# Performance work log

Hardware: AMD Instinct MI355X
Metric: run time of the kernel (lower is better)

Reference implementation:

```python
import jax, jax.numpy as jnp
import numpy as np

DIM = 1024
LATENT_DIM = 512
NUM_HEADS = 16
HEAD_DIM = DIM // NUM_HEADS
SCALE = HEAD_DIM ** -0.5


def setup_inputs() -> dict:
    key = jax.random.key(0)
    k1, k2, k3, k4, k5 = jax.random.split(key, 5)
    B, xN, zN = 2, 2048, 2048
    x = jax.random.normal(k1, (B, xN, DIM), dtype=jnp.float32)
    z = jax.random.normal(k2, (B, zN, LATENT_DIM), dtype=jnp.float32)
    # torch Linear weights: [out_features, in_features]
    Wq = jax.random.normal(k3, (DIM, DIM), dtype=jnp.float32) * (DIM ** -0.5)
    Wkv = jax.random.normal(k4, (2 * DIM, LATENT_DIM), dtype=jnp.float32) * (LATENT_DIM ** -0.5)
    Wo = jax.random.normal(k5, (DIM, DIM), dtype=jnp.float32) * (DIM ** -0.5)
    return {"x": x, "z": z, "Wq": Wq, "Wkv": Wkv, "Wo": Wo}


def reference(x, z, Wq, Wkv, Wo):
    B, xN, _ = x.shape
    _, zN, _ = z.shape
    # projections (torch Linear: y = x @ W.T)
    Q = (x @ Wq.T).reshape(B, xN, NUM_HEADS, HEAD_DIM)        # [B,xN,H,D]
    KV = (z @ Wkv.T).reshape(B, zN, 2, NUM_HEADS, HEAD_DIM)   # [B,zN,2,H,D]
    K = KV[:, :, 0]                                            # [B,zN,H,D]
    V = KV[:, :, 1]
    attn = jnp.einsum('bqhd,bkhd->bhqk', Q, K) * SCALE         # [B,H,xN,zN]
    attn = jax.nn.softmax(attn, axis=-1)
    O = jnp.einsum('bhqk,bkhd->bqhd', attn, V).reshape(B, xN, DIM)
    return O @ Wo.T
```

## Files before the change

### kernel.cpp

```cpp
#include <hip/hip_runtime.h>
#include <stdint.h>

#define SEQ 2048
#define QSCALE 0.1803368801111244f
#define DEFER_THR 11.5f

typedef __attribute__((ext_vector_type(8))) short bf16x8;
typedef __attribute__((ext_vector_type(4))) short bf16x4;
typedef __attribute__((ext_vector_type(4))) float f32x4;
typedef __attribute__((ext_vector_type(16))) float f32x16;
typedef unsigned short u16;

__device__ __forceinline__ u16 f2bf(float f) {
  union { float f; uint32_t u; } v; v.f = f;
  uint32_t u = v.u;
  u += 0x7fffu + ((u >> 16) & 1u);
  return (u16)(u >> 16);
}

__device__ __forceinline__ float fast_exp2(float x) {
#if __has_builtin(__builtin_amdgcn_exp2f)
  return __builtin_amdgcn_exp2f(x);
#else
  return exp2f(x);
#endif
}

__device__ __forceinline__ uint32_t cvtpk(float a, float b) {
  uint32_t r;
  asm("v_cvt_pk_bf16_f32 %0, %1, %2" : "=v"(r) : "v"(a), "v"(b));
  return r;
}

__device__ __forceinline__ void swap_pair(uint32_t& a, uint32_t& b, int hi) {
  uint32_t ta = (uint32_t)__shfl_xor((int)a, 32);
  uint32_t tb = (uint32_t)__shfl_xor((int)b, 32);
  a = hi ? tb : a;
  b = hi ? b : ta;
}

__device__ __forceinline__ void gload_lds16(const u16* g, u16* l) {
  __builtin_amdgcn_global_load_lds((__attribute__((address_space(1))) void*)g,
                                   (__attribute__((address_space(3))) void*)l,
                                   16, 0, 0);
}

__global__ void cvt5_kernel(const float* __restrict__ x, const float* __restrict__ z,
                            const float* __restrict__ Wq, const float* __restrict__ Wkv,
                            const float* __restrict__ Wo,
                            u16* __restrict__ xb, u16* __restrict__ zb,
                            u16* __restrict__ wqb, u16* __restrict__ wkvb,
                            u16* __restrict__ wob) {
  const int X4 = 1048576, Z4 = 524288, W4 = 262144;
  const int total = X4 + Z4 + 3 * W4;
  int i = blockIdx.x * blockDim.x + threadIdx.x;
  const int stride = gridDim.x * blockDim.x;
  for (; i < total; i += stride) {
    const float* src; u16* dst; int j = i;
    if (j < X4)              { src = x;   dst = xb; }
    else if ((j -= X4) < Z4) { src = z;   dst = zb; }
    else if ((j -= Z4) < W4) { src = Wq;  dst = wqb; }
    else if ((j -= W4) < W4) { src = Wkv; dst = wkvb; }
    else       { j -= W4;      src = Wo;  dst = wob; }
    float4 v = ((const float4*)src)[j];
    bf16x4 o;
    o[0] = (short)f2bf(v.x); o[1] = (short)f2bf(v.y);
    o[2] = (short)f2bf(v.z); o[3] = (short)f2bf(v.w);
    ((bf16x4*)dst)[j] = o;
  }
}

template <int BN, typename CT>
__device__ __forceinline__ void gemm64_body(const u16* __restrict__ A,
                                            const u16* __restrict__ B,
                                            CT* __restrict__ C,
                                            int N, int K, float scale,
                                            int tm, int tn, u16* As, u16* Bs) {
  constexpr int NB = BN / 32;
  const int tid = threadIdx.x;
  const int wid = tid >> 6;
  const int lane = tid & 63;
  const int lg = lane >> 4, lq = lane & 15;
  const int wr = wid >> 1, wc = wid & 1;

  f32x4 acc[4][NB];
#pragma unroll
  for (int m = 0; m < 4; m++)
#pragma unroll
    for (int n = 0; n < NB; n++)
#pragma unroll
      for (int e = 0; e < 4; e++) acc[m][n][e] = 0.f;

  const int r0 = tid >> 3;
  const int c0 = tid & 7;
  const int sc = (c0 ^ (r0 & 7)) * 8;
  const u16* gA = A + (size_t)(tm * 128 + r0) * K + sc;
  const u16* gB = B + (size_t)(tn * BN + r0) * K + sc;
  u16* lA = As + wid * 512;
  u16* lB = Bs + wid * 512;

  for (int k0 = 0; k0 < K; k0 += 64) {
    __syncthreads();
#pragma unroll
    for (int i = 0; i < 4; i++)
      gload_lds16(gA + k0 + (size_t)(32 * i) * K, lA + i * 2048);
#pragma unroll
    for (int i = 0; i < NB; i++)
      gload_lds16(gB + k0 + (size_t)(32 * i) * K, lB + i * 2048);
    __syncthreads();

#pragma unroll
    for (int ks = 0; ks < 2; ks++) {
      const int slot = ((ks * 4 + lg) ^ (lq & 7)) * 8;
      bf16x8 af[4], bfr[NB];
#pragma unroll
      for (int m = 0; m < 4; m++)
        af[m] = *(const bf16x8*)(As + (wr * 64 + m * 16 + lq) * 64 + slot);
#pragma unroll
      for (int n = 0; n < NB; n++)
        bfr[n] = *(const bf16x8*)(Bs + (wc * (BN / 2) + n * 16 + lq) * 64 + slot);
#pragma unroll
      for (int m = 0; m < 4; m++)
#pragma unroll
        for (int n = 0; n < NB; n++)
          acc[m][n] = __builtin_amdgcn_mfma_f32_16x16x32_bf16(af[m], bfr[n], acc[m][n], 0, 0, 0);
    }
  }

#pragma unroll
  for (int m = 0; m < 4; m++) {
    const int row = tm * 128 + wr * 64 + m * 16 + lg * 4;
#pragma unroll
    for (int i = 0; i < 4; i++) {
      CT* cp = C + (size_t)(row + i) * N + tn * BN + wc * (BN / 2) + lq;
#pragma unroll
      for (int n = 0; n < NB; n++) {
        float v = acc[m][n][i] * scale;
        if constexpr (sizeof(CT) == 2) cp[n * 16] = (CT)f2bf(v);
        else                            cp[n * 16] = (CT)v;
      }
    }
  }
}

__global__ __launch_bounds__(256, 3) void qkv_gemm(const u16* __restrict__ xb,
                                                   const u16* __restrict__ zb,
                                                   const u16* __restrict__ Wqb,
                                                   const u16* __restrict__ Wkvb,
                                                   u16* __restrict__ Qb,
                                                   u16* __restrict__ Kb,
                                                   u16* __restrict__ VTb) {
  __shared__ __align__(16) u16 As[128 * 64];
  __shared__ __align__(16) u16 Bs[128 * 64];
  const int bi = blockIdx.x;
  int g = (bi & 7) * 96 + (bi >> 3);
  if (g < 256) {
    gemm64_body<128, u16>(xb, Wqb, Qb, 1024, 1024, QSCALE, g >> 3, g & 7, As, Bs);
  } else if (g < 512) {
    g -= 256;
    gemm64_body<128, u16>(zb, Wkvb, Kb, 1024, 512, 1.f, g >> 3, g & 7, As, Bs);
  } else {
    g -= 512;
    gemm64_body<128, u16>(Wkvb + 1024 * 512, zb, VTb, 4096, 512, 1.f, g >> 5, g & 31, As, Bs);
  }
}

__global__ __launch_bounds__(256) void combine_kernel(const u16* __restrict__ OP,
                                                      const float2* __restrict__ ml,
                                                      u16* __restrict__ Ob) {
  const int i = blockIdx.x * 256 + threadIdx.x;
  const int grow = i >> 7;
  const int h = (i >> 3) & 15;
  const float2 a0 = ml[grow * 16 + h];
  const float2 a1 = ml[4096 * 16 + grow * 16 + h];
  const float M = fmaxf(a0.x, a1.x);
  float w0 = a0.y * fast_exp2(a0.x - M);
  float w1 = a1.y * fast_exp2(a1.x - M);
  const float inv = 1.f / (w0 + w1);
  w0 *= inv; w1 *= inv;
  const bf16x8 p0 = ((const bf16x8*)OP)[i];
  const bf16x8 p1 = ((const bf16x8*)(OP + (size_t)4096 * 1024))[i];
  bf16x8 o;
#pragma unroll
  for (int e = 0; e < 8; e++) {
    union { uint32_t u; float f; } f0, f1;
    f0.u = ((uint32_t)(u16)p0[e]) << 16;
    f1.u = ((uint32_t)(u16)p1[e]) << 16;
    o[e] = (short)f2bf(w0 * f0.f + w1 * f1.f);
  }
  ((bf16x8*)Ob)[i] = o;
}

__global__ __launch_bounds__(256) void o_gemm(const u16* __restrict__ Ob,
                                              const u16* __restrict__ Wob,
                                              float* __restrict__ out) {
  __shared__ __align__(16) u16 As[128 * 64];
  __shared__ __align__(16) u16 Bs[64 * 64];
  const int bi = blockIdx.x;
  const int xcd = bi & 7, j = bi >> 3;
  const int tm = xcd * 4 + (j >> 4);
  const int tn = j & 15;
  gemm64_body<64, float>(Ob, Wob, out, 1024, 1024, 1.f, tm, tn, As, Bs);
}

__global__ __launch_bounds__(256, 4) void attn_kernel(const u16* __restrict__ Q,
                                                      const u16* __restrict__ K,
                                                      const u16* __restrict__ VT,
                                                      u16* __restrict__ OP,
                                                      float2* __restrict__ ml) {
  __shared__ __align__(16) u16 LDS[16384];

  const int tid = threadIdx.x;
  const int wid = tid >> 6;
  const int lane = tid & 63;
  const int l31 = lane & 31;
  const int hi = lane >> 5;

  const int bi = blockIdx.x;
  const int xcd = bi & 7, j = bi >> 3;
  const int qt = j & 15;
  const int s  = (j >> 4) & 1;
  const int bh = xcd + 8 * (j >> 5);
  const int b = bh >> 4, h = bh & 15;
  const int t0 = s * 16;

  const int q0 = qt * 128 + wid * 32;

  bf16x8 qf[4];
  {
    const u16* qp = Q + (size_t)(b * SEQ + q0 + l31) * 1024 + h * 64 + hi * 8;
#pragma unroll
    for (int ks = 0; ks < 4; ks++) qf[ks] = *(const bf16x8*)(qp + ks * 16);
  }

  f32x16 of[2];
#pragma unroll
  for (int d = 0; d < 2; d++)
#pragma unroll
    for (int e = 0; e < 16; e++) of[d][e] = 0.f;
  float m_run = -3.0e38f, l_run = 0.f;

  const char* rdB[4];
#pragma unroll
  for (int ks = 0; ks < 4; ks++)
    rdB[ks] = (const char*)LDS + l31 * 128 + ((((2 * ks + hi) ^ (lane & 7))) << 4);

  const int r0 = tid >> 3;
  const int srcc = ((tid & 7) ^ (r0 & 7)) << 3;
  const u16* gK = K + (size_t)(b * SEQ + r0) * 1024 + h * 64 + srcc;
  const u16* gV = VT + (size_t)(h * 64 + r0) * 4096 + b * SEQ + srcc;
  u16* lK = LDS + wid * 512;
  u16* lV = LDS + 8192 + wid * 512;

  auto stage = [&](int t, int buf) {
    const u16* sk = gK + (size_t)t * 64 * 1024;
    gload_lds16(sk, lK + buf * 4096);
    gload_lds16(sk + (size_t)32 * 1024, lK + buf * 4096 + 2048);
    const u16* sv = gV + t * 64;
    gload_lds16(sv, lV + buf * 4096);
    gload_lds16(sv + (size_t)32 * 4096, lV + buf * 4096 + 2048);
  };

  auto tile_compute = [&](int buf) {
    const int bo = buf * 8192;

    f32x16 sacc[2];
#pragma unroll
    for (int kb = 0; kb < 2; kb++)
#pragma unroll
      for (int e = 0; e < 16; e++) sacc[kb][e] = 0.f;
    __builtin_amdgcn_s_setprio(1);
#pragma unroll
    for (int kb = 0; kb < 2; kb++)
#pragma unroll
      for (int ks = 0; ks < 4; ks++) {
        bf16x8 kf = *(const bf16x8*)(rdB[ks] + bo + kb * 4096);
        sacc[kb] = __builtin_amdgcn_mfma_f32_32x32x16_bf16(kf, qf[ks], sacc[kb], 0, 0, 0);
      }
    __builtin_amdgcn_s_setprio(0);

    float a0 = sacc[0][0], a1 = sacc[0][1], a2 = sacc[0][2], a3 = sacc[0][3];
#pragma unroll
    for (int e = 4; e < 16; e += 4) {
      a0 = fmaxf(a0, sacc[0][e]);     a1 = fmaxf(a1, sacc[0][e + 1]);
      a2 = fmaxf(a2, sacc[0][e + 2]); a3 = fmaxf(a3, sacc[0][e + 3]);
    }
#pragma unroll
    for (int e = 0; e < 16; e += 4) {
      a0 = fmaxf(a0, sacc[1][e]);     a1 = fmaxf(a1, sacc[1][e + 1]);
      a2 = fmaxf(a2, sacc[1][e + 2]); a3 = fmaxf(a3, sacc[1][e + 3]);
    }
    float tmax = fmaxf(fmaxf(a0, a1), fmaxf(a2, a3));
    tmax = fmaxf(tmax, __shfl_xor(tmax, 32));

    if (!__all(tmax <= m_run + DEFER_THR)) {
      const float m_new = fmaxf(m_run, tmax);
      const float esc = fast_exp2(m_run - m_new);
      l_run *= esc;
#pragma unroll
      for (int r = 0; r < 16; r++) {
        const int qof = (r & 3) + 8 * (r >> 2) + 4 * hi;
        const float e = __shfl(esc, qof);
        of[0][r] *= e;
        of[1][r] *= e;
      }
      m_run = m_new;
    }

    float s0 = 0.f, s1 = 0.f, s2 = 0.f, s3 = 0.f;
#pragma unroll
    for (int kb = 0; kb < 2; kb++)
#pragma unroll
      for (int e = 0; e < 16; e += 4) {
        float p0 = fast_exp2(sacc[kb][e] - m_run);
        float p1 = fast_exp2(sacc[kb][e + 1] - m_run);
        float p2 = fast_exp2(sacc[kb][e + 2] - m_run);
        float p3 = fast_exp2(sacc[kb][e + 3] - m_run);
        sacc[kb][e] = p0; sacc[kb][e + 1] = p1; sacc[kb][e + 2] = p2; sacc[kb][e + 3] = p3;
        s0 += p0; s1 += p1; s2 += p2; s3 += p3;
      }
    l_run += (s0 + s1) + (s2 + s3);

    bf16x8 pa[4];
#pragma unroll
    for (int kb = 0; kb < 2; kb++) {
      uint32_t c0 = cvtpk(sacc[kb][0],  sacc[kb][1]);
      uint32_t c1 = cvtpk(sacc[kb][2],  sacc[kb][3]);
      uint32_t c2 = cvtpk(sacc[kb][4],  sacc[kb][5]);
      uint32_t c3 = cvtpk(sacc[kb][6],  sacc[kb][7]);
      uint32_t c4 = cvtpk(sacc[kb][8],  sacc[kb][9]);
      uint32_t c5 = cvtpk(sacc[kb][10], sacc[kb][11]);
      uint32_t c6 = cvtpk(sacc[kb][12], sacc[kb][13]);
      uint32_t c7 = cvtpk(sacc[kb][14], sacc[kb][15]);
      swap_pair(c0, c2, hi);
      swap_pair(c1, c3, hi);
      swap_pair(c4, c6, hi);
      swap_pair(c5, c7, hi);
      union { bf16x8 v; uint32_t d[4]; } u0, u1;
      u0.d[0] = c0; u0.d[1] = c1; u0.d[2] = c2; u0.d[3] = c3;
      u1.d[0] = c4; u1.d[1] = c5; u1.d[2] = c6; u1.d[3] = c7;
      pa[2 * kb] = u0.v;
      pa[2 * kb + 1] = u1.v;
    }

    __builtin_amdgcn_s_setprio(1);
#pragma unroll
    for (int ks = 0; ks < 4; ks++)
#pragma unroll
      for (int db = 0; db < 2; db++) {
        bf16x8 vf = *(const bf16x8*)(rdB[ks] + bo + 16384 + db * 4096);
        of[db] = __builtin_amdgcn_mfma_f32_32x32x16_bf16(pa[ks], vf, of[db], 0, 0, 0);
      }
    __builtin_amdgcn_s_setprio(0);
  };

  stage(t0, 0);
  __syncthreads();
#pragma unroll 1
  for (int tt = 0; tt < 16; tt += 2) {
    stage(t0 + tt + 1, 1);
    tile_compute(0);
    __syncthreads();
    if (tt < 14) stage(t0 + tt + 2, 0);
    tile_compute(1);
    __syncthreads();
  }

  const float lsum = l_run + __shfl_xor(l_run, 32);
  const float linv = 1.f / lsum;

  u16* OPs = OP + (size_t)s * 4096 * 1024;
#pragma unroll
  for (int r = 0; r < 16; r++) {
    const int qof = (r & 3) + 8 * (r >> 2) + 4 * hi;
    const float li = __shfl(linv, qof);
    u16* op = OPs + (size_t)(b * SEQ + q0 + qof) * 1024 + h * 64 + l31;
    op[0]  = f2bf(of[0][r] * li);
    op[32] = f2bf(of[1][r] * li);
  }
  if (hi == 0) {
    const int grow = b * SEQ + q0 + l31;
    ml[s * (4096 * 16) + grow * 16 + h] = make_float2(m_run, lsum);
  }
}

extern "C" void kernel_launch(void* const* d_in, const int* in_sizes, int n_in,
                              void* d_out, int out_size, void* d_ws, size_t ws_size,
                              hipStream_t stream) {
  const float* x   = (const float*)d_in[0];
  const float* z   = (const float*)d_in[1];
  const float* Wq  = (const float*)d_in[2];
  const float* Wkv = (const float*)d_in[3];
  const float* Wo  = (const float*)d_in[4];
  float* out = (float*)d_out;

  char* ws = (char*)d_ws;
  const size_t MB = 1024ull * 1024ull;
  u16* xb   = (u16*)(ws + 0);
  u16* zb   = (u16*)(ws + 8 * MB);
  u16* Wqb  = (u16*)(ws + 12 * MB);
  u16* Wkvb = (u16*)(ws + 14 * MB);
  u16* Wob  = (u16*)(ws + 16 * MB);
  u16* Qb   = (u16*)(ws + 18 * MB);
  u16* Kb   = (u16*)(ws + 26 * MB);
  u16* VTb  = (u16*)(ws + 34 * MB);
  u16* Ob   = (u16*)(ws + 42 * MB);
  u16* OP   = (u16*)(ws + 0);
  float2* ml = (float2*)(ws + 50 * MB);

  cvt5_kernel<<<2048, 256, 0, stream>>>(x, z, Wq, Wkv, Wo, xb, zb, Wqb, Wkvb, Wob);

  qkv_gemm<<<768, 256, 0, stream>>>(xb, zb, Wqb, Wkvb, Qb, Kb, VTb);

  attn_kernel<<<1024, 256, 0, stream>>>(Qb, Kb, VTb, OP, ml);

  combine_kernel<<<2048, 256, 0, stream>>>(OP, ml, Ob);

  o_gemm<<<512, 256, 0, stream>>>(Ob, Wob, out);
}
```

Before: 117.5 us.

## Load K and V fragments directly from global memory instead of LDS staging

Removes the shared-memory double-buffered staging of K and V tiles, along with its barriers, in the attention kernel. Each wave now reads its K and V MFMA operand fragments straight from global memory on every tile. The aim is to drop LDS traffic and __syncthreads stalls. In exchange, the four waves of a block each reload the same K/V data, with no software prefetch and exposed global latency before each MFMA.

```diff
diff --git a/kernel.cpp b/kernel.cpp
--- a/kernel.cpp
+++ b/kernel.cpp
@@ -208,8 +208,6 @@
                                                       const u16* __restrict__ VT,
                                                       u16* __restrict__ OP,
                                                       float2* __restrict__ ml) {
-  __shared__ __align__(16) u16 LDS[16384];
-
   const int tid = threadIdx.x;
   const int wid = tid >> 6;
   const int lane = tid & 63;
@@ -240,29 +238,17 @@
     for (int e = 0; e < 16; e++) of[d][e] = 0.f;
   float m_run = -3.0e38f, l_run = 0.f;
 
-  const char* rdB[4];
-#pragma unroll
-  for (int ks = 0; ks < 4; ks++)
-    rdB[ks] = (const char*)LDS + l31 * 128 + ((((2 * ks + hi) ^ (lane & 7))) << 4);
-
-  const int r0 = tid >> 3;
-  const int srcc = ((tid & 7) ^ (r0 & 7)) << 3;
-  const u16* gK = K + (size_t)(b * SEQ + r0) * 1024 + h * 64 + srcc;
-  const u16* gV = VT + (size_t)(h * 64 + r0) * 4096 + b * SEQ + srcc;
-  u16* lK = LDS + wid * 512;
-  u16* lV = LDS + 8192 + wid * 512;
-
-  auto stage = [&](int t, int buf) {
-    const u16* sk = gK + (size_t)t * 64 * 1024;
-    gload_lds16(sk, lK + buf * 4096);
-    gload_lds16(sk + (size_t)32 * 1024, lK + buf * 4096 + 2048);
-    const u16* sv = gV + t * 64;
-    gload_lds16(sv, lV + buf * 4096);
-    gload_lds16(sv + (size_t)32 * 4096, lV + buf * 4096 + 2048);
-  };
-
-  auto tile_compute = [&](int buf) {
-    const int bo = buf * 8192;
+  const u16* kp = K + (size_t)(b * SEQ + t0 * 64 + l31) * 1024 + h * 64 + hi * 8;
+  const u16* vp = VT + (size_t)(h * 64 + l31) * 4096 + b * SEQ + t0 * 64 + hi * 8;
+
+#pragma unroll 1
+  for (int tt = 0; tt < 16; ++tt) {
+    bf16x8 kf0[4], kf1[4];
+#pragma unroll
+    for (int ks = 0; ks < 4; ks++) {
+      kf0[ks] = *(const bf16x8*)(kp + ks * 16);
+      kf1[ks] = *(const bf16x8*)(kp + (size_t)32 * 1024 + ks * 16);
+    }
 
     f32x16 sacc[2];
 #pragma unroll
@@ -271,12 +257,11 @@
       for (int e = 0; e < 16; e++) sacc[kb][e] = 0.f;
     __builtin_amdgcn_s_setprio(1);
 #pragma unroll
-    for (int kb = 0; kb < 2; kb++)
-#pragma unroll
-      for (int ks = 0; ks < 4; ks++) {
-        bf16x8 kf = *(const bf16x8*)(rdB[ks] + bo + kb * 4096);
-        sacc[kb] = __builtin_amdgcn_mfma_f32_32x32x16_bf16(kf, qf[ks], sacc[kb], 0, 0, 0);
-      }
+    for (int ks = 0; ks < 4; ks++)
+      sacc[0] = __builtin_amdgcn_mfma_f32_32x32x16_bf16(kf0[ks], qf[ks], sacc[0], 0, 0, 0);
+#pragma unroll
+    for (int ks = 0; ks < 4; ks++)
+      sacc[1] = __builtin_amdgcn_mfma_f32_32x32x16_bf16(kf1[ks], qf[ks], sacc[1], 0, 0, 0);
     __builtin_amdgcn_s_setprio(0);
 
     float a0 = sacc[0][0], a1 = sacc[0][1], a2 = sacc[0][2], a3 = sacc[0][3];
@@ -345,25 +330,16 @@
 
     __builtin_amdgcn_s_setprio(1);
 #pragma unroll
-    for (int ks = 0; ks < 4; ks++)
-#pragma unroll
-      for (int db = 0; db < 2; db++) {
-        bf16x8 vf = *(const bf16x8*)(rdB[ks] + bo + 16384 + db * 4096);
-        of[db] = __builtin_amdgcn_mfma_f32_32x32x16_bf16(pa[ks], vf, of[db], 0, 0, 0);
-      }
+    for (int ks = 0; ks < 4; ks++) {
+      bf16x8 v0 = *(const bf16x8*)(vp + ks * 16);
+      bf16x8 v1 = *(const bf16x8*)(vp + (size_t)32 * 4096 + ks * 16);
+      of[0] = __builtin_amdgcn_mfma_f32_32x32x16_bf16(pa[ks], v0, of[0], 0, 0, 0);
+      of[1] = __builtin_amdgcn_mfma_f32_32x32x16_bf16(pa[ks], v1, of[1], 0, 0, 0);
+    }
     __builtin_amdgcn_s_setprio(0);
-  };
-
-  stage(t0, 0);
-  __syncthreads();
-#pragma unroll 1
-  for (int tt = 0; tt < 16; tt += 2) {
-    stage(t0 + tt + 1, 1);
-    tile_compute(0);
-    __syncthreads();
-    if (tt < 14) stage(t0 + tt + 2, 0);
-    tile_compute(1);
-    __syncthreads();
+
+    kp += 64 * 1024;
+    vp += 64;
   }
 
   const float lsum = l_run + __shfl_xor(l_run, 32);
```

After: 184.5 us. 1.57x slower.
